# Optimization experiments

Hardware: AMD Instinct MI355X
Metric: run time of the kernel (lower is better)

The kernel has to match this reference:

```python
import jax, jax.numpy as jnp
import numpy as np

EPS = 0.001  # additive floor applied after relu, as in the torch code


def setup_inputs() -> dict:
    key = jax.random.key(0)
    kA, kB, kW = jax.random.split(key, 3)
    M, N, C, H, W = 512, 64, 128, 8, 8
    A = jax.random.normal(kA, (M, C, H, W), dtype=jnp.float32)
    B = jax.random.normal(kB, (N, C, H, W), dtype=jnp.float32)
    Wg = jax.random.normal(kW, (C, C), dtype=jnp.float32) * 0.01  # Wg.data.normal_(0.0, 0.01)
    return {"A": A, "B": B, "Wg": Wg}


def reference(A, B, Wg):
    # Faithful vectorization of MIMOcom.get_source_dst_max(A, B, dir=True).
    # Torch loops i,j over HxW: B0 = B[:, i, j, :]; G = B0 @ Wg;
    # combination[m, n, p] = sum_c A[m, p, c] * G[n, c]; running max over (i, j).
    M, C, H, W = A.shape
    N = B.shape[0]
    P = H * W
    Af = jnp.transpose(A, (0, 2, 3, 1)).reshape(M, P, C)  # [M, P, C]
    Bf = jnp.transpose(B, (0, 2, 3, 1)).reshape(N, P, C)  # [N, Q, C]
    G = Bf @ Wg                                           # [N, Q, D]
    scores = jnp.einsum('mpd,nqd->mnpq', Af, G)           # [M, N, P, Q]
    comb_max = scores.max(axis=-1)                        # max over B positions q
    return jax.nn.relu(comb_max) + EPS                    # [M, N, P]
```

## Files before the change

### kernel.cpp

```cpp
#include <hip/hip_runtime.h>
#include <hip/hip_bf16.h>
#include <stdint.h>

typedef __attribute__((ext_vector_type(8))) short bf16x8;
typedef __attribute__((ext_vector_type(16))) float f32x16;
using bf16 = __hip_bfloat16;

static constexpr int Mdim = 512;
static constexpr int Ndim = 64;
static constexpr int Cdim = 128;
static constexpr int Pdim = 64;
static constexpr float EPS_ADD = 0.001f;

#define SB0 __builtin_amdgcn_sched_barrier(0)
#define WAITV(N) asm volatile("s_waitcnt vmcnt(" #N ")" ::: "memory")

__device__ __forceinline__ void gll16(const void* gsrc, void* ldst) {
    const __attribute__((address_space(1))) unsigned int* g =
        (const __attribute__((address_space(1))) unsigned int*)gsrc;
    __attribute__((address_space(3))) unsigned int* l =
        (__attribute__((address_space(3))) unsigned int*)(uintptr_t)ldst;
    __builtin_amdgcn_global_load_lds(g, l, 16, 0, 0);
}

__global__ void prep_kernel(const float* __restrict__ A, const float* __restrict__ B,
                            const float* __restrict__ Wg,
                            bf16* __restrict__ Afrag, bf16* __restrict__ Gfrag) {
    __shared__ float lds[128 * 65];
    const int t = threadIdx.x;

    if (blockIdx.x < 512) {
        const int m = blockIdx.x;
        const float* __restrict__ Am = A + (size_t)m * (Cdim * Pdim);
#pragma unroll
        for (int i = 0; i < 8; ++i) {
            int v = t + i * 256;
            int gidx = v * 4;
            int c = gidx >> 6, p = gidx & 63;
            float4 val = *reinterpret_cast<const float4*>(Am + gidx);
            float* dst = &lds[c * 65 + p];
            dst[0] = val.x; dst[1] = val.y; dst[2] = val.z; dst[3] = val.w;
        }
        __syncthreads();

        unsigned* __restrict__ dst32 = (unsigned*)(Afrag + (size_t)m * 8192);
#pragma unroll
        for (int i = 0; i < 16; ++i) {
            int pr = t + i * 256;
            int p = pr >> 6;
            int c = (pr & 63) << 1;
            float f0 = lds[c * 65 + p];
            float f1 = lds[(c + 1) * 65 + p];
            union { bf16 hh[2]; unsigned u; } pk;
            pk.hh[0] = __float2bfloat16(f0);
            pk.hh[1] = __float2bfloat16(f1);
            int h = p >> 5, l31 = p & 31;
            int ks = c >> 4, hi = (c >> 3) & 1, e = c & 7;
            dst32[h * 2048 + ks * 256 + hi * 128 + l31 * 4 + (e >> 1)] = pk.u;
        }
    } else {
        const int nb = blockIdx.x - 512;
        const int n  = nb >> 2;
        const int q0 = (nb & 3) * 16;
        const float* __restrict__ Bn = B + (size_t)n * (Cdim * Pdim);
#pragma unroll
        for (int i = 0; i < 8; ++i) {
            int v = t + i * 256;
            int gidx = v * 4;
            int c = gidx >> 6, q = gidx & 63;
            float4 val = *reinterpret_cast<const float4*>(Bn + gidx);
            float* dst = &lds[c * 65 + q];
            dst[0] = val.x; dst[1] = val.y; dst[2] = val.z; dst[3] = val.w;
        }
        __syncthreads();

        const int d  = t & 127;
        const int qb = q0 + (t >> 7) * 8;
        float acc[8] = {0.f, 0.f, 0.f, 0.f, 0.f, 0.f, 0.f, 0.f};
        for (int c = 0; c < 128; ++c) {
            float w = Wg[c * 128 + d];
#pragma unroll
            for (int qi = 0; qi < 8; ++qi)
                acc[qi] = fmaf(lds[c * 65 + qb + qi], w, acc[qi]);
        }
        bf16* __restrict__ gdst = Gfrag + (size_t)n * 8192;
        const int ks = d >> 4, hi = (d >> 3) & 1, e = d & 7;
#pragma unroll
        for (int qi = 0; qi < 8; ++qi) {
            int q = qb + qi;
            int qt = q >> 5, l31 = q & 31;
            gdst[qt * 4096 + ks * 512 + hi * 256 + l31 * 8 + e] = __float2bfloat16(acc[qi]);
        }
    }
}

__global__ __launch_bounds__(256, 2)
void gemm_max_kernel(const bf16* __restrict__ Afrag, const bf16* __restrict__ Gfrag,
                     float* __restrict__ out) {
    __shared__ bf16 sG[4][8192];
    const int tid  = threadIdx.x;
    const int lane = tid & 63;
    const int wv   = tid >> 6;
    const int l31 = lane & 31, hi = lane >> 5;
    const int mg = blockIdx.x & 127;
    const int bn = blockIdx.x >> 7;
    const int m  = mg * 4 + wv;

    bf16x8 a[2][8];
    {
        const bf16* Ap = Afrag + (size_t)m * 8192 + lane * 8;
#pragma unroll
        for (int h = 0; h < 2; ++h)
#pragma unroll
            for (int ks = 0; ks < 8; ++ks)
                a[h][ks] = *reinterpret_cast<const bf16x8*>(Ap + h * 4096 + ks * 512);
    }
    asm volatile("" ::: "memory");

    const char* Gsrc = (const char*)(Gfrag + (size_t)(bn * 16) * 8192);
    auto stageG = [&](int s) {
        char* dst = (char*)&sG[s & 3][0];
        const char* src = Gsrc + (size_t)s * 16384;
#pragma unroll
        for (int i = 0; i < 4; ++i) {
            int f = (i * 256 + tid) * 16;
            gll16(src + f, dst + f);
        }
    };
    stageG(0);
    stageG(1);

    f32x16 acc[2][2];
    const f32x16 z16 = {0.f,0.f,0.f,0.f,0.f,0.f,0.f,0.f,0.f,0.f,0.f,0.f,0.f,0.f,0.f,0.f};

    auto compute = [&](int s) {
        const char* gb = (const char*)&sG[s & 3][0] + lane * 16;
        bf16x8 gf[2][8];
#pragma unroll
        for (int qt = 0; qt < 2; ++qt)
#pragma unroll
            for (int ks = 0; ks < 8; ++ks)
                gf[qt][ks] = *reinterpret_cast<const bf16x8*>(gb + qt * 8192 + ks * 1024);
        __builtin_amdgcn_s_setprio(1);
#pragma unroll
        for (int ks = 0; ks < 8; ++ks)
#pragma unroll
            for (int qt = 0; qt < 2; ++qt)
#pragma unroll
                for (int h = 0; h < 2; ++h)
                    acc[qt][h] = __builtin_amdgcn_mfma_f32_32x32x16_bf16(
                        gf[qt][ks], a[h][ks], ks == 0 ? z16 : acc[qt][h], 0, 0, 0);
        __builtin_amdgcn_s_setprio(0);
    };

    auto epilogue = [&](int s) {
        const int ng = bn * 16 + s;
#pragma unroll
        for (int h = 0; h < 2; ++h) {
            float v = fmaxf(acc[0][h][0], acc[0][h][1]);
#pragma unroll
            for (int j = 2; j < 16; ++j) v = fmaxf(v, acc[0][h][j]);
#pragma unroll
            for (int j = 0; j < 16; ++j) v = fmaxf(v, acc[1][h][j]);
            v = fmaxf(v, __shfl_xor(v, 32));
            if (hi == 0)
                out[(size_t)m * 4096 + ng * 64 + h * 32 + l31] = fmaxf(v, 0.f) + EPS_ADD;
        }
    };

    WAITV(4); __builtin_amdgcn_s_barrier(); SB0;
    stageG(2); compute(0); epilogue(0); SB0;

    WAITV(6); __builtin_amdgcn_s_barrier(); SB0;
    stageG(3); compute(1); epilogue(1); SB0;

    for (int s = 2; s <= 13; ++s) {
        WAITV(8); __builtin_amdgcn_s_barrier(); SB0;
        stageG(s + 2); compute(s); epilogue(s); SB0;
    }

    WAITV(8); __builtin_amdgcn_s_barrier(); SB0;
    compute(14); epilogue(14); SB0;

    WAITV(4); __builtin_amdgcn_s_barrier(); SB0;
    compute(15); epilogue(15);
}

extern "C" void kernel_launch(void* const* d_in, const int* in_sizes, int n_in,
                              void* d_out, int out_size, void* d_ws, size_t ws_size,
                              hipStream_t stream) {
    const float* A  = (const float*)d_in[0];
    const float* B  = (const float*)d_in[1];
    const float* Wg = (const float*)d_in[2];
    float* out = (float*)d_out;

    bf16* Afrag = (bf16*)d_ws;
    bf16* Gfrag = (bf16*)((char*)d_ws + (size_t)Mdim * Pdim * Cdim * sizeof(bf16));

    prep_kernel<<<768, 256, 0, stream>>>(A, B, Wg, Afrag, Gfrag);
    gemm_max_kernel<<<512, 256, 0, stream>>>(Afrag, Gfrag, out);
}
```

Baseline: 47.02 us.

## Split GEMM-max work across more blocks and raise occupancy with a 3-stage ring

The grid doubles to 1024 blocks, each covering 8 N-groups instead of 16. Each wave now owns one P-half for two M rows, so a single G fragment feeds two MFMAs. G fragments are loaded per k-step rather than all 16 at once, and only two accumulators stay live. Together with a 3-buffer LDS ring, this lowers register and LDS pressure enough to allow 3 blocks per CU. The goal is better latency hiding and fuller CU coverage, at the risk of LDS loads stalling the MFMA chain because they are interleaved instead of prefetched.

```diff
diff --git a/kernel.cpp b/kernel.cpp
--- a/kernel.cpp
+++ b/kernel.cpp
@@ -94,32 +94,34 @@
     }
 }
 
-__global__ __launch_bounds__(256, 2)
+__global__ __launch_bounds__(256, 3)
 void gemm_max_kernel(const bf16* __restrict__ Afrag, const bf16* __restrict__ Gfrag,
                      float* __restrict__ out) {
-    __shared__ bf16 sG[4][8192];
+    __shared__ bf16 sG[3][8192];
     const int tid  = threadIdx.x;
     const int lane = tid & 63;
     const int wv   = tid >> 6;
+    const int mi = wv >> 1, h = wv & 1;
     const int l31 = lane & 31, hi = lane >> 5;
     const int mg = blockIdx.x & 127;
     const int bn = blockIdx.x >> 7;
-    const int m  = mg * 4 + wv;
+    const int m0 = mg * 4 + mi * 2;
 
     bf16x8 a[2][8];
     {
-        const bf16* Ap = Afrag + (size_t)m * 8192 + lane * 8;
-#pragma unroll
-        for (int h = 0; h < 2; ++h)
+#pragma unroll
+        for (int u = 0; u < 2; ++u) {
+            const bf16* Ap = Afrag + (size_t)(m0 + u) * 8192 + h * 4096 + lane * 8;
 #pragma unroll
             for (int ks = 0; ks < 8; ++ks)
-                a[h][ks] = *reinterpret_cast<const bf16x8*>(Ap + h * 4096 + ks * 512);
+                a[u][ks] = *reinterpret_cast<const bf16x8*>(Ap + ks * 512);
+        }
     }
     asm volatile("" ::: "memory");
 
-    const char* Gsrc = (const char*)(Gfrag + (size_t)(bn * 16) * 8192);
+    const char* Gsrc = (const char*)(Gfrag + (size_t)(bn * 8) * 8192);
     auto stageG = [&](int s) {
-        char* dst = (char*)&sG[s & 3][0];
+        char* dst = (char*)&sG[s % 3][0];
         const char* src = Gsrc + (size_t)s * 16384;
 #pragma unroll
         for (int i = 0; i < 4; ++i) {
@@ -130,60 +132,58 @@
     stageG(0);
     stageG(1);
 
-    f32x16 acc[2][2];
     const f32x16 z16 = {0.f,0.f,0.f,0.f,0.f,0.f,0.f,0.f,0.f,0.f,0.f,0.f,0.f,0.f,0.f,0.f};
 
-    auto compute = [&](int s) {
-        const char* gb = (const char*)&sG[s & 3][0] + lane * 16;
-        bf16x8 gf[2][8];
-#pragma unroll
-        for (int qt = 0; qt < 2; ++qt)
-#pragma unroll
-            for (int ks = 0; ks < 8; ++ks)
-                gf[qt][ks] = *reinterpret_cast<const bf16x8*>(gb + qt * 8192 + ks * 1024);
-        __builtin_amdgcn_s_setprio(1);
-#pragma unroll
-        for (int ks = 0; ks < 8; ++ks)
-#pragma unroll
-            for (int qt = 0; qt < 2; ++qt)
-#pragma unroll
-                for (int h = 0; h < 2; ++h)
-                    acc[qt][h] = __builtin_amdgcn_mfma_f32_32x32x16_bf16(
-                        gf[qt][ks], a[h][ks], ks == 0 ? z16 : acc[qt][h], 0, 0, 0);
-        __builtin_amdgcn_s_setprio(0);
+    auto step = [&](int s) {
+        const char* gb = (const char*)&sG[s % 3][0] + lane * 16;
+        float r0, r1;
+#pragma unroll
+        for (int qt = 0; qt < 2; ++qt) {
+            f32x16 acc0, acc1;
+            __builtin_amdgcn_s_setprio(1);
+#pragma unroll
+            for (int ks = 0; ks < 8; ++ks) {
+                bf16x8 gf = *reinterpret_cast<const bf16x8*>(gb + qt * 8192 + ks * 1024);
+                acc0 = __builtin_amdgcn_mfma_f32_32x32x16_bf16(
+                    gf, a[0][ks], ks == 0 ? z16 : acc0, 0, 0, 0);
+                acc1 = __builtin_amdgcn_mfma_f32_32x32x16_bf16(
+                    gf, a[1][ks], ks == 0 ? z16 : acc1, 0, 0, 0);
+            }
+            __builtin_amdgcn_s_setprio(0);
+            float t0 = fmaxf(acc0[0], acc0[1]);
+#pragma unroll
+            for (int j = 2; j < 16; ++j) t0 = fmaxf(t0, acc0[j]);
+            float t1 = fmaxf(acc1[0], acc1[1]);
+#pragma unroll
+            for (int j = 2; j < 16; ++j) t1 = fmaxf(t1, acc1[j]);
+            if (qt == 0) { r0 = t0; r1 = t1; }
+            else         { r0 = fmaxf(r0, t0); r1 = fmaxf(r1, t1); }
+        }
+        r0 = fmaxf(r0, __shfl_xor(r0, 32));
+        r1 = fmaxf(r1, __shfl_xor(r1, 32));
+        const int n = bn * 8 + s;
+        if (hi == 0) {
+            out[(size_t)m0 * 4096 + n * 64 + h * 32 + l31]       = fmaxf(r0, 0.f) + EPS_ADD;
+            out[(size_t)(m0 + 1) * 4096 + n * 64 + h * 32 + l31] = fmaxf(r1, 0.f) + EPS_ADD;
+        }
     };
 
-    auto epilogue = [&](int s) {
-        const int ng = bn * 16 + s;
-#pragma unroll
-        for (int h = 0; h < 2; ++h) {
-            float v = fmaxf(acc[0][h][0], acc[0][h][1]);
-#pragma unroll
-            for (int j = 2; j < 16; ++j) v = fmaxf(v, acc[0][h][j]);
-#pragma unroll
-            for (int j = 0; j < 16; ++j) v = fmaxf(v, acc[1][h][j]);
-            v = fmaxf(v, __shfl_xor(v, 32));
-            if (hi == 0)
-                out[(size_t)m * 4096 + ng * 64 + h * 32 + l31] = fmaxf(v, 0.f) + EPS_ADD;
-        }
-    };
-
     WAITV(4); __builtin_amdgcn_s_barrier(); SB0;
-    stageG(2); compute(0); epilogue(0); SB0;
+    stageG(2); step(0); SB0;
 
     WAITV(6); __builtin_amdgcn_s_barrier(); SB0;
-    stageG(3); compute(1); epilogue(1); SB0;
-
-    for (int s = 2; s <= 13; ++s) {
+    stageG(3); step(1); SB0;
+
+    for (int s = 2; s <= 5; ++s) {
         WAITV(8); __builtin_amdgcn_s_barrier(); SB0;
-        stageG(s + 2); compute(s); epilogue(s); SB0;
+        stageG(s + 2); step(s); SB0;
     }
 
     WAITV(8); __builtin_amdgcn_s_barrier(); SB0;
-    compute(14); epilogue(14); SB0;
+    step(6); SB0;
 
     WAITV(4); __builtin_amdgcn_s_barrier(); SB0;
-    compute(15); epilogue(15);
+    step(7);
 }
 
 extern "C" void kernel_launch(void* const* d_in, const int* in_sizes, int n_in,
@@ -198,5 +198,5 @@
     bf16* Gfrag = (bf16*)((char*)d_ws + (size_t)Mdim * Pdim * Cdim * sizeof(bf16));
 
     prep_kernel<<<768, 256, 0, stream>>>(A, B, Wg, Afrag, Gfrag);
-    gemm_max_kernel<<<512, 256, 0, stream>>>(Afrag, Gfrag, out);
-}
+    gemm_max_kernel<<<1024, 256, 0, stream>>>(Afrag, Gfrag, out);
+}
```

New measurement: 45.70 us. 2.8% less time.
